# Kernel tuning notes

Measured on AMD Instinct MI355X. Metric: run time of the kernel, lower is better.

The kernel has to match this reference:

```python
import jax, jax.numpy as jnp
import numpy as np

DIM = 128
LAYERS = 3
N_NODES = 50000
N_EDGES = 640000
LN_EPS = 1e-5


def setup_inputs() -> dict:
    key = jax.random.key(0)
    ks = jax.random.split(key, 10)
    s = 1.0 / np.sqrt(DIM)
    x = jax.random.normal(ks[0], (N_NODES, DIM), dtype=jnp.float32)
    edge_index = jax.random.randint(ks[1], (2, N_EDGES), 0, N_NODES, dtype=jnp.int64)
    in_w = jax.random.uniform(ks[2], (DIM, DIM), jnp.float32, -s, s)
    in_b = jax.random.uniform(ks[3], (DIM,), jnp.float32, -s, s)
    w1 = jax.random.uniform(ks[4], (LAYERS, DIM, DIM), jnp.float32, -s, s)
    b1 = jax.random.uniform(ks[5], (LAYERS, DIM), jnp.float32, -s, s)
    w2 = jax.random.uniform(ks[6], (LAYERS, DIM, DIM), jnp.float32, -s, s)
    b2 = jax.random.uniform(ks[7], (LAYERS, DIM), jnp.float32, -s, s)
    ln_g = jnp.ones((LAYERS, DIM), jnp.float32)
    ln_b = jnp.zeros((LAYERS, DIM), jnp.float32)
    return {"x": x, "edge_index": edge_index, "in_w": in_w, "in_b": in_b,
            "w1": w1, "b1": b1, "w2": w2, "b2": b2, "ln_g": ln_g, "ln_b": ln_b}


def _layer_norm(z, g, b):
    mu = jnp.mean(z, axis=-1, keepdims=True)
    var = jnp.mean(jnp.square(z - mu), axis=-1, keepdims=True)
    return (z - mu) * jax.lax.rsqrt(var + LN_EPS) * g + b


def reference(x, edge_index, in_w, in_b, w1, b1, w2, b2, ln_g, ln_b):
    src, dst = edge_index[0], edge_index[1]
    n = x.shape[0]
    # degree is identical every layer in the original; compute once (same math)
    deg = jax.ops.segment_sum(jnp.ones(dst.shape, x.dtype), dst, num_segments=n)
    deg = jnp.maximum(deg, 1.0)[:, None]  # [N,1]
    h = x @ in_w + in_b  # [N,D]
    for i in range(w1.shape[0]):
        m = jax.ops.segment_sum(h[src], dst, num_segments=n) / deg  # gather+scatter
        mlp = jax.nn.relu(m @ w1[i] + b1[i]) @ w2[i] + b2[i]
        h = _layer_norm(h + mlp, ln_g[i], ln_b[i])
    return h
```

## Files before the change

kernel.cpp:

```cpp
#include <hip/hip_runtime.h>
#include <hip/hip_fp8.h>

#define DIM 128
#define LN_EPS 1e-5f
#define ECAP 512

typedef __attribute__((ext_vector_type(8))) short s16x8;
typedef __attribute__((ext_vector_type(4))) float f32x4;
typedef __attribute__((ext_vector_type(2))) float f32x2;
typedef __attribute__((ext_vector_type(4))) unsigned int u32x4;
typedef __attribute__((ext_vector_type(2))) unsigned int u32x2;

__device__ __forceinline__ unsigned short f2bf(float f) {
    unsigned u = __float_as_uint(f);
    unsigned r = u + 0x7fffu + ((u >> 16) & 1u);
    return (unsigned short)(r >> 16);
}
__device__ __forceinline__ float bf2f(unsigned short b) {
    return __uint_as_float(((unsigned)b) << 16);
}
__device__ __forceinline__ unsigned char f2fp8(float f) {
    return (unsigned char)__hip_cvt_float_to_fp8(f, __HIP_SATFINITE, __HIP_E4M3);
}
__device__ __forceinline__ void acc_fp8x4(float* a, unsigned v) {
    f32x2 lo = __builtin_amdgcn_cvt_pk_f32_fp8(v, false);
    f32x2 hi = __builtin_amdgcn_cvt_pk_f32_fp8(v, true);
    a[0] += lo[0]; a[1] += lo[1]; a[2] += hi[0]; a[3] += hi[1];
}


__global__ void count_deg(const int* __restrict__ dst, int E, int* __restrict__ counts) {
    int i = blockIdx.x * 256 + threadIdx.x;
    if (i < E) atomicAdd(&counts[dst[i]], 1);
}

__global__ __launch_bounds__(256) void scan_partials(const int* __restrict__ counts, int n,
                                                     int* __restrict__ bsum) {
    int base = blockIdx.x * 1024 + threadIdx.x * 4;
    int s = 0;
#pragma unroll
    for (int j = 0; j < 4; ++j) {
        int i = base + j;
        if (i < n) s += counts[i];
    }
#pragma unroll
    for (int off = 32; off > 0; off >>= 1) s += __shfl_xor(s, off, 64);
    __shared__ int wsum[4];
    int lane = threadIdx.x & 63, wid = threadIdx.x >> 6;
    if (lane == 0) wsum[wid] = s;
    __syncthreads();
    if (threadIdx.x == 0) bsum[blockIdx.x] = wsum[0] + wsum[1] + wsum[2] + wsum[3];
}

__global__ __launch_bounds__(64) void scan_bsums(const int* __restrict__ bsum,
                                                 int* __restrict__ bofs, int nb,
                                                 int* __restrict__ rowptr, int N, int E) {
    int lane = threadIdx.x;
    int carry = 0;
    for (int base = 0; base < nb; base += 64) {
        int v = (base + lane < nb) ? bsum[base + lane] : 0;
        int incl = v;
#pragma unroll
        for (int off = 1; off < 64; off <<= 1) {
            int t = __shfl_up(incl, off, 64);
            if (lane >= off) incl += t;
        }
        if (base + lane < nb) bofs[base + lane] = carry + incl - v;
        carry += __shfl(incl, 63, 64);
    }
    if (lane == 0) rowptr[N] = E;
}

__global__ __launch_bounds__(256) void scan_final(const int* __restrict__ counts, int n,
                                                  const int* __restrict__ bofs,
                                                  int* __restrict__ rowptr,
                                                  int* __restrict__ cursor,
                                                  float* __restrict__ dinv) {
    int base = blockIdx.x * 1024 + threadIdx.x * 4;
    int v[4];
#pragma unroll
    for (int j = 0; j < 4; ++j) {
        int i = base + j;
        v[j] = (i < n) ? counts[i] : 0;
    }
    int tsum = v[0] + v[1] + v[2] + v[3];
    int lane = threadIdx.x & 63, wid = threadIdx.x >> 6;
    int incl = tsum;
#pragma unroll
    for (int off = 1; off < 64; off <<= 1) {
        int t = __shfl_up(incl, off, 64);
        if (lane >= off) incl += t;
    }
    __shared__ int wsum[4];
    if (lane == 63) wsum[wid] = incl;
    __syncthreads();
    int wofs = 0;
    for (int w = 0; w < 4; ++w)
        if (w < wid) wofs += wsum[w];
    int excl = bofs[blockIdx.x] + wofs + (incl - tsum);
#pragma unroll
    for (int j = 0; j < 4; ++j) {
        int i = base + j;
        if (i < n) {
            rowptr[i] = excl;
            cursor[i] = excl;
            dinv[i] = 1.0f / (float)((v[j] > 1) ? v[j] : 1);
            excl += v[j];
        }
    }
}

__global__ void fill_csr(const int* __restrict__ src, const int* __restrict__ dst, int E,
                         int* __restrict__ cursor, int* __restrict__ srcidx) {
    int i = blockIdx.x * 256 + threadIdx.x;
    if (i < E) {
        int p = atomicAdd(&cursor[dst[i]], 1);
        srcidx[p] = src[i];
    }
}


__global__ __launch_bounds__(256) void cvt_weights(const float* __restrict__ in_w,
                                                   const float* __restrict__ w1,
                                                   const float* __restrict__ w2,
                                                   unsigned short* __restrict__ wt, int L) {
    int mat = blockIdx.x >> 3, part = blockIdx.x & 7;
    const float* src;
    if (mat == 0) src = in_w;
    else if (mat <= L) src = w1 + (size_t)(mat - 1) * DIM * DIM;
    else src = w2 + (size_t)(mat - 1 - L) * DIM * DIM;
    unsigned short* dst = wt + (size_t)mat * DIM * DIM;
    int base = part * 2048 + threadIdx.x;
#pragma unroll
    for (int j = 0; j < 8; ++j) {
        int i = base + j * 256;
        int k = i >> 7, n = i & 127;
        dst[n * DIM + k] = f2bf(src[i]);
    }
}


__global__ __launch_bounds__(256) void gemm_bias_mfma(const float* __restrict__ x,
                                                      const unsigned short* __restrict__ Wt,
                                                      const float* __restrict__ bias,
                                                      unsigned short* __restrict__ hb,
                                                      unsigned char* __restrict__ h8, int N) {
    int tid = threadIdx.x;
    int s = tid >> 6, lane = tid & 63;
    int quad = lane >> 4, l16 = lane & 15;
    int r0 = blockIdx.x * 16;
    int cs = s * 32;
    int arow = r0 + l16;
    bool av = arow < N;

    f32x4 acc[2];
    acc[0] = (f32x4){0.f, 0.f, 0.f, 0.f};
    acc[1] = (f32x4){0.f, 0.f, 0.f, 0.f};

    const float4* xp = (const float4*)(x + ((size_t)(av ? arow : 0) << 7)) + quad * 2;
#pragma unroll
    for (int k0 = 0; k0 < 128; k0 += 32) {
        s16x8 a = {0, 0, 0, 0, 0, 0, 0, 0};
        if (av) {
            float4 f0 = xp[k0 / 4];
            float4 f1 = xp[k0 / 4 + 1];
            a[0] = (short)f2bf(f0.x); a[1] = (short)f2bf(f0.y);
            a[2] = (short)f2bf(f0.z); a[3] = (short)f2bf(f0.w);
            a[4] = (short)f2bf(f1.x); a[5] = (short)f2bf(f1.y);
            a[6] = (short)f2bf(f1.z); a[7] = (short)f2bf(f1.w);
        }
        s16x8 b0 = *(const s16x8*)(Wt + ((size_t)(cs + l16) << 7) + quad * 8 + k0);
        s16x8 b1 = *(const s16x8*)(Wt + ((size_t)(cs + 16 + l16) << 7) + quad * 8 + k0);
        acc[0] = __builtin_amdgcn_mfma_f32_16x16x32_bf16(a, b0, acc[0], 0, 0, 0);
        acc[1] = __builtin_amdgcn_mfma_f32_16x16x32_bf16(a, b1, acc[1], 0, 0, 0);
    }

#pragma unroll
    for (int c = 0; c < 2; ++c) {
        int col = cs + c * 16 + l16;
        float bv = bias[col];
#pragma unroll
        for (int reg = 0; reg < 4; ++reg) {
            int grow = r0 + quad * 4 + reg;
            if (grow < N) {
                float o = acc[c][reg] + bv;
                hb[((size_t)grow << 7) + col] = f2bf(o);
                h8[((size_t)grow << 7) + col] = f2fp8(o);
            }
        }
    }
}


__global__ __launch_bounds__(256) void agg_mlp_ln(const unsigned short* __restrict__ hin,
                                                  const unsigned char* __restrict__ h8in,
                                                  const int* __restrict__ rowptr,
                                                  const int* __restrict__ srcidx,
                                                  const float* __restrict__ dinv,
                                                  const unsigned short* __restrict__ W1t,
                                                  const float* __restrict__ B1,
                                                  const unsigned short* __restrict__ W2t,
                                                  const float* __restrict__ B2,
                                                  const float* __restrict__ G,
                                                  const float* __restrict__ Bb,
                                                  unsigned short* __restrict__ hout,
                                                  unsigned char* __restrict__ h8out,
                                                  float* __restrict__ out_f32, int N) {
    __shared__ unsigned short M[16][132];
    __shared__ unsigned short P[16][132];
    __shared__ float s1p[4][16], s2p[4][16];
    __shared__ int eL[ECAP];
    __shared__ int rp[17];

    int tid = threadIdx.x;
    int s = tid >> 6, lane = tid & 63;
    int quad = lane >> 4, l16 = lane & 15;
    int g = lane >> 2, li = lane & 3;
    int r0 = blockIdx.x * 16;
    int cs = s * 32;

    if (tid < 17) {
        int idx = r0 + tid;
        rp[tid] = rowptr[idx < N ? idx : N];
    }
    __syncthreads();
    int ebase = rp[0];
    int etot = rp[16] - ebase;
    int estg = etot < ECAP ? etot : ECAP;
    for (int i = tid; i < estg; i += 256) eL[i] = srcidx[ebase + i];
    __syncthreads();

    int nd = r0 + g;
    bool nv = nd < N;
    int ls = rp[g] - ebase;
    int le = rp[g + 1] - ebase;
    if (!nv) { ls = 0; le = 0; }
    float di = nv ? dinv[nd] : 0.f;

    const unsigned char* hsl = h8in + cs + li * 8;

    float a0[8] = {0, 0, 0, 0, 0, 0, 0, 0};
    float a1[8] = {0, 0, 0, 0, 0, 0, 0, 0};

#define LIDX(jj) (((jj) < le) ? (((jj) < ECAP) ? eL[(jj)] : srcidx[ebase + (jj)]) : -1)

    int jA = ls;
    int iA0 = LIDX(jA + 0), iA1 = LIDX(jA + 1), iA2 = LIDX(jA + 2), iA3 = LIDX(jA + 3);
    u32x2 A0 = {0, 0}, A1 = {0, 0}, A2 = {0, 0}, A3 = {0, 0};
    if (iA0 >= 0) A0 = *(const u32x2*)(hsl + ((size_t)iA0 << 7));
    if (iA1 >= 0) A1 = *(const u32x2*)(hsl + ((size_t)iA1 << 7));
    if (iA2 >= 0) A2 = *(const u32x2*)(hsl + ((size_t)iA2 << 7));
    if (iA3 >= 0) A3 = *(const u32x2*)(hsl + ((size_t)iA3 << 7));
    int jB = jA + 4;
    int iB0 = LIDX(jB + 0), iB1 = LIDX(jB + 1), iB2 = LIDX(jB + 2), iB3 = LIDX(jB + 3);

    while (__any(jA < le)) {
        u32x2 B0 = {0, 0}, B1v = {0, 0}, B2v = {0, 0}, B3 = {0, 0};
        if (iB0 >= 0) B0  = *(const u32x2*)(hsl + ((size_t)iB0 << 7));
        if (iB1 >= 0) B1v = *(const u32x2*)(hsl + ((size_t)iB1 << 7));
        if (iB2 >= 0) B2v = *(const u32x2*)(hsl + ((size_t)iB2 << 7));
        if (iB3 >= 0) B3  = *(const u32x2*)(hsl + ((size_t)iB3 << 7));
        int jC = jB + 4;
        int iC0 = LIDX(jC + 0), iC1 = LIDX(jC + 1), iC2 = LIDX(jC + 2), iC3 = LIDX(jC + 3);
        acc_fp8x4(a0, A0[0]); acc_fp8x4(a0 + 4, A0[1]);
        acc_fp8x4(a1, A1[0]); acc_fp8x4(a1 + 4, A1[1]);
        acc_fp8x4(a0, A2[0]); acc_fp8x4(a0 + 4, A2[1]);
        acc_fp8x4(a1, A3[0]); acc_fp8x4(a1 + 4, A3[1]);
        jA = jB; A0 = B0; A1 = B1v; A2 = B2v; A3 = B3;
        jB = jC; iB0 = iC0; iB1 = iC1; iB2 = iC2; iB3 = iC3;
    }
#undef LIDX

    {
        u32x4 o;
#pragma unroll
        for (int j = 0; j < 4; ++j) {
            unsigned lo = f2bf((a0[2 * j]     + a1[2 * j])     * di);
            unsigned hi = f2bf((a0[2 * j + 1] + a1[2 * j + 1]) * di);
            o[j] = lo | (hi << 16);
        }
        *(u32x4*)(&M[g][cs + li * 8]) = o;
    }
    __syncthreads();

    unsigned short hvr[2][4];
#pragma unroll
    for (int c = 0; c < 2; ++c) {
        int col = cs + c * 16 + l16;
#pragma unroll
        for (int reg = 0; reg < 4; ++reg) {
            int grow = r0 + quad * 4 + reg;
            hvr[c][reg] = (grow < N) ? hin[((size_t)grow << 7) + col] : (unsigned short)0;
        }
    }

    f32x4 acc[2];
    acc[0] = (f32x4){0.f, 0.f, 0.f, 0.f};
    acc[1] = (f32x4){0.f, 0.f, 0.f, 0.f};
#pragma unroll
    for (int k0 = 0; k0 < 128; k0 += 32) {
        s16x8 a = *(const s16x8*)(&M[l16][quad * 8 + k0]);
        s16x8 b0 = *(const s16x8*)(W1t + ((size_t)(cs + l16) << 7) + quad * 8 + k0);
        s16x8 b1 = *(const s16x8*)(W1t + ((size_t)(cs + 16 + l16) << 7) + quad * 8 + k0);
        acc[0] = __builtin_amdgcn_mfma_f32_16x16x32_bf16(a, b0, acc[0], 0, 0, 0);
        acc[1] = __builtin_amdgcn_mfma_f32_16x16x32_bf16(a, b1, acc[1], 0, 0, 0);
    }
#pragma unroll
    for (int c = 0; c < 2; ++c) {
        int col = cs + c * 16 + l16;
        float bv = B1[col];
#pragma unroll
        for (int reg = 0; reg < 4; ++reg) {
            float v = fmaxf(acc[c][reg] + bv, 0.f);
            P[quad * 4 + reg][col] = f2bf(v);
        }
    }
    __syncthreads();

    acc[0] = (f32x4){0.f, 0.f, 0.f, 0.f};
    acc[1] = (f32x4){0.f, 0.f, 0.f, 0.f};
#pragma unroll
    for (int k0 = 0; k0 < 128; k0 += 32) {
        s16x8 a = *(const s16x8*)(&P[l16][quad * 8 + k0]);
        s16x8 b0 = *(const s16x8*)(W2t + ((size_t)(cs + l16) << 7) + quad * 8 + k0);
        s16x8 b1 = *(const s16x8*)(W2t + ((size_t)(cs + 16 + l16) << 7) + quad * 8 + k0);
        acc[0] = __builtin_amdgcn_mfma_f32_16x16x32_bf16(a, b0, acc[0], 0, 0, 0);
        acc[1] = __builtin_amdgcn_mfma_f32_16x16x32_bf16(a, b1, acc[1], 0, 0, 0);
    }

    float z[2][4];
    float ps1[4] = {0, 0, 0, 0}, ps2[4] = {0, 0, 0, 0};
#pragma unroll
    for (int c = 0; c < 2; ++c) {
        int col = cs + c * 16 + l16;
        float b2v = B2[col];
#pragma unroll
        for (int reg = 0; reg < 4; ++reg) {
            float hv = bf2f(hvr[c][reg]);
            float zz = acc[c][reg] + b2v + hv;
            z[c][reg] = zz;
            ps1[reg] += zz;
            ps2[reg] += zz * zz;
        }
    }
#pragma unroll
    for (int off = 1; off < 16; off <<= 1) {
#pragma unroll
        for (int reg = 0; reg < 4; ++reg) {
            ps1[reg] += __shfl_xor(ps1[reg], off, 64);
            ps2[reg] += __shfl_xor(ps2[reg], off, 64);
        }
    }
    if (l16 == 0) {
#pragma unroll
        for (int reg = 0; reg < 4; ++reg) {
            s1p[s][quad * 4 + reg] = ps1[reg];
            s2p[s][quad * 4 + reg] = ps2[reg];
        }
    }
    __syncthreads();

#pragma unroll
    for (int reg = 0; reg < 4; ++reg) {
        int row = quad * 4 + reg;
        float S1 = s1p[0][row] + s1p[1][row] + s1p[2][row] + s1p[3][row];
        float S2 = s2p[0][row] + s2p[1][row] + s2p[2][row] + s2p[3][row];
        float mean = S1 * (1.0f / 128.0f);
        float var = S2 * (1.0f / 128.0f) - mean * mean;
        float rs = rsqrtf(var + LN_EPS);
        int grow = r0 + row;
        if (grow < N) {
#pragma unroll
            for (int c = 0; c < 2; ++c) {
                int col = cs + c * 16 + l16;
                float o = (z[c][reg] - mean) * rs * G[col] + Bb[col];
                if (out_f32) {
                    out_f32[((size_t)grow << 7) + col] = o;
                } else {
                    hout[((size_t)grow << 7) + col] = f2bf(o);
                    h8out[((size_t)grow << 7) + col] = f2fp8(o);
                }
            }
        }
    }
}


extern "C" void kernel_launch(void* const* d_in, const int* in_sizes, int n_in,
                              void* d_out, int out_size, void* d_ws, size_t ws_size,
                              hipStream_t stream) {
    const float* x    = (const float*)d_in[0];
    const int*   ei   = (const int*)d_in[1];
    const float* in_w = (const float*)d_in[2];
    const float* in_b = (const float*)d_in[3];
    const float* w1   = (const float*)d_in[4];
    const float* b1   = (const float*)d_in[5];
    const float* w2   = (const float*)d_in[6];
    const float* b2   = (const float*)d_in[7];
    const float* ln_g = (const float*)d_in[8];
    const float* ln_b = (const float*)d_in[9];

    const int N = in_sizes[0] / DIM;
    const int E = in_sizes[1] / 2;
    const int LAYERS = in_sizes[4] / (DIM * DIM);

    const int* e_src = ei;
    const int* e_dst = ei + E;

    char* ws = (char*)d_ws;
    unsigned short* hb0    = (unsigned short*)ws;  ws += (size_t)N * DIM * 2;
    unsigned short* hb1    = (unsigned short*)ws;  ws += (size_t)N * DIM * 2;
    unsigned char*  h8a    = (unsigned char*)ws;   ws += (size_t)N * DIM;
    unsigned char*  h8b    = (unsigned char*)ws;   ws += (size_t)N * DIM;
    int*            counts = (int*)ws;             ws += (size_t)N * 4;
    int*            rowptr = (int*)ws;             ws += (size_t)(N + 1) * 4;
    int*            cursor = (int*)ws;             ws += (size_t)N * 4;
    float*          dinv   = (float*)ws;           ws += (size_t)N * 4;
    int*            srcidx = (int*)ws;             ws += (size_t)E * 4;
    int*            bsum   = (int*)ws;             ws += 4096;
    int*            bofs   = (int*)ws;             ws += 4096;
    unsigned short* wt     = (unsigned short*)ws;  ws += (size_t)(2 * LAYERS + 1) * DIM * DIM * 2;

    const int nScanBlocks = (N + 1023) / 1024;
    const int nMat = 2 * LAYERS + 1;

    (void)hipMemsetAsync(counts, 0, (size_t)N * 4, stream);
    count_deg<<<(E + 255) / 256, 256, 0, stream>>>(e_dst, E, counts);
    scan_partials<<<nScanBlocks, 256, 0, stream>>>(counts, N, bsum);
    scan_bsums<<<1, 64, 0, stream>>>(bsum, bofs, nScanBlocks, rowptr, N, E);
    scan_final<<<nScanBlocks, 256, 0, stream>>>(counts, N, bofs, rowptr, cursor, dinv);
    fill_csr<<<(E + 255) / 256, 256, 0, stream>>>(e_src, e_dst, E, cursor, srcidx);
    cvt_weights<<<nMat * 8, 256, 0, stream>>>(in_w, w1, w2, wt, LAYERS);

    const unsigned short* in_wt = wt;
    const unsigned short* w1t   = wt + (size_t)DIM * DIM;
    const unsigned short* w2t   = wt + (size_t)(1 + LAYERS) * DIM * DIM;

    int tile_grid = (N + 15) / 16;
    gemm_bias_mfma<<<tile_grid, 256, 0, stream>>>(x, in_wt, in_b, hb0, h8a, N);

    unsigned short* hin  = hb0;  unsigned char* h8in  = h8a;
    unsigned short* hout = hb1;  unsigned char* h8out = h8b;
    for (int i = 0; i < LAYERS; ++i) {
        float* out = (i == LAYERS - 1) ? (float*)d_out : nullptr;
        agg_mlp_ln<<<tile_grid, 256, 0, stream>>>(hin, h8in, rowptr, srcidx, dinv,
                                                  w1t + (size_t)i * DIM * DIM, b1 + (size_t)i * DIM,
                                                  w2t + (size_t)i * DIM * DIM, b2 + (size_t)i * DIM,
                                                  ln_g + (size_t)i * DIM, ln_b + (size_t)i * DIM,
                                                  hout, h8out, out, N);
        unsigned short* t = hin; hin = hout; hout = t;
        unsigned char* t8 = h8in; h8in = h8out; h8out = t8;
    }
}
```

Measured before the change: 353.8 us.

## Process 32 rows per block in fused aggregate-MLP-LN kernel with wider gathers

The fused aggregation+MLP+LayerNorm kernel now handles 32 node rows per block instead of 16. Each wave gathers 8 nodes, with 8 lanes per node loading 16-byte fp8 chunks, replacing the old scheme of 4 lanes per node loading 8 bytes. Each wave runs two 16-row MFMA tiles per weight fragment, so every W1/W2 fragment load is reused twice, and the shared edge-index staging capacity grows. Separately, the degree-count and CSR-fill kernels now process four edges per thread with int4 loads. This trades more registers and LDS per block, and fewer blocks, for better weight reuse and wider memory transactions.

```diff
diff --git a/kernel.cpp b/kernel.cpp
--- a/kernel.cpp
+++ b/kernel.cpp
@@ -3,7 +3,7 @@
 
 #define DIM 128
 #define LN_EPS 1e-5f
-#define ECAP 512
+#define ECAP 640
 
 typedef __attribute__((ext_vector_type(8))) short s16x8;
 typedef __attribute__((ext_vector_type(4))) float f32x4;
@@ -27,11 +27,25 @@
     f32x2 hi = __builtin_amdgcn_cvt_pk_f32_fp8(v, true);
     a[0] += lo[0]; a[1] += lo[1]; a[2] += hi[0]; a[3] += hi[1];
 }
+__device__ __forceinline__ void acc_fp8x16(float* a, u32x4 v) {
+    acc_fp8x4(a + 0,  v[0]);
+    acc_fp8x4(a + 4,  v[1]);
+    acc_fp8x4(a + 8,  v[2]);
+    acc_fp8x4(a + 12, v[3]);
+}
 
 
 __global__ void count_deg(const int* __restrict__ dst, int E, int* __restrict__ counts) {
-    int i = blockIdx.x * 256 + threadIdx.x;
-    if (i < E) atomicAdd(&counts[dst[i]], 1);
+    int i = (blockIdx.x * 256 + threadIdx.x) * 4;
+    if (i + 3 < E) {
+        int4 d = *(const int4*)(dst + i);
+        atomicAdd(&counts[d.x], 1);
+        atomicAdd(&counts[d.y], 1);
+        atomicAdd(&counts[d.z], 1);
+        atomicAdd(&counts[d.w], 1);
+    } else {
+        for (int j = i; j < E; ++j) atomicAdd(&counts[dst[j]], 1);
+    }
 }
 
 __global__ __launch_bounds__(256) void scan_partials(const int* __restrict__ counts, int n,
@@ -112,10 +126,19 @@
 
 __global__ void fill_csr(const int* __restrict__ src, const int* __restrict__ dst, int E,
                          int* __restrict__ cursor, int* __restrict__ srcidx) {
-    int i = blockIdx.x * 256 + threadIdx.x;
-    if (i < E) {
-        int p = atomicAdd(&cursor[dst[i]], 1);
-        srcidx[p] = src[i];
+    int i = (blockIdx.x * 256 + threadIdx.x) * 4;
+    if (i + 3 < E) {
+        int4 s = *(const int4*)(src + i);
+        int4 d = *(const int4*)(dst + i);
+        int p0 = atomicAdd(&cursor[d.x], 1); srcidx[p0] = s.x;
+        int p1 = atomicAdd(&cursor[d.y], 1); srcidx[p1] = s.y;
+        int p2 = atomicAdd(&cursor[d.z], 1); srcidx[p2] = s.z;
+        int p3 = atomicAdd(&cursor[d.w], 1); srcidx[p3] = s.w;
+    } else {
+        for (int j = i; j < E; ++j) {
+            int p = atomicAdd(&cursor[dst[j]], 1);
+            srcidx[p] = src[j];
+        }
     }
 }
 
@@ -206,179 +229,211 @@
                                                   unsigned short* __restrict__ hout,
                                                   unsigned char* __restrict__ h8out,
                                                   float* __restrict__ out_f32, int N) {
-    __shared__ unsigned short M[16][132];
-    __shared__ unsigned short P[16][132];
-    __shared__ float s1p[4][16], s2p[4][16];
+    __shared__ unsigned short M[32][132];
+    __shared__ unsigned short P[32][132];
+    __shared__ float s1p[4][32], s2p[4][32];
     __shared__ int eL[ECAP];
-    __shared__ int rp[17];
+    __shared__ int rp[33];
 
     int tid = threadIdx.x;
-    int s = tid >> 6, lane = tid & 63;
+    int w = tid >> 6, lane = tid & 63;
     int quad = lane >> 4, l16 = lane & 15;
-    int g = lane >> 2, li = lane & 3;
-    int r0 = blockIdx.x * 16;
-    int cs = s * 32;
-
-    if (tid < 17) {
+    int g = lane >> 3, li = lane & 7;
+    int r0 = blockIdx.x * 32;
+    int cs = w * 32;
+
+    if (tid < 33) {
         int idx = r0 + tid;
         rp[tid] = rowptr[idx < N ? idx : N];
     }
     __syncthreads();
     int ebase = rp[0];
-    int etot = rp[16] - ebase;
+    int etot = rp[32] - ebase;
     int estg = etot < ECAP ? etot : ECAP;
     for (int i = tid; i < estg; i += 256) eL[i] = srcidx[ebase + i];
     __syncthreads();
 
-    int nd = r0 + g;
+    int nrow = w * 8 + g;
+    int nd = r0 + nrow;
     bool nv = nd < N;
-    int ls = rp[g] - ebase;
-    int le = rp[g + 1] - ebase;
+    int ls = rp[nrow] - ebase;
+    int le = rp[nrow + 1] - ebase;
     if (!nv) { ls = 0; le = 0; }
     float di = nv ? dinv[nd] : 0.f;
 
-    const unsigned char* hsl = h8in + cs + li * 8;
-
-    float a0[8] = {0, 0, 0, 0, 0, 0, 0, 0};
-    float a1[8] = {0, 0, 0, 0, 0, 0, 0, 0};
+    const unsigned char* hsl = h8in + li * 16;
+
+    float a[16];
+#pragma unroll
+    for (int j = 0; j < 16; ++j) a[j] = 0.f;
 
 #define LIDX(jj) (((jj) < le) ? (((jj) < ECAP) ? eL[(jj)] : srcidx[ebase + (jj)]) : -1)
 
     int jA = ls;
     int iA0 = LIDX(jA + 0), iA1 = LIDX(jA + 1), iA2 = LIDX(jA + 2), iA3 = LIDX(jA + 3);
-    u32x2 A0 = {0, 0}, A1 = {0, 0}, A2 = {0, 0}, A3 = {0, 0};
-    if (iA0 >= 0) A0 = *(const u32x2*)(hsl + ((size_t)iA0 << 7));
-    if (iA1 >= 0) A1 = *(const u32x2*)(hsl + ((size_t)iA1 << 7));
-    if (iA2 >= 0) A2 = *(const u32x2*)(hsl + ((size_t)iA2 << 7));
-    if (iA3 >= 0) A3 = *(const u32x2*)(hsl + ((size_t)iA3 << 7));
+    u32x4 A0 = {0, 0, 0, 0}, A1 = {0, 0, 0, 0}, A2 = {0, 0, 0, 0}, A3 = {0, 0, 0, 0};
+    if (iA0 >= 0) A0 = *(const u32x4*)(hsl + ((size_t)iA0 << 7));
+    if (iA1 >= 0) A1 = *(const u32x4*)(hsl + ((size_t)iA1 << 7));
+    if (iA2 >= 0) A2 = *(const u32x4*)(hsl + ((size_t)iA2 << 7));
+    if (iA3 >= 0) A3 = *(const u32x4*)(hsl + ((size_t)iA3 << 7));
     int jB = jA + 4;
     int iB0 = LIDX(jB + 0), iB1 = LIDX(jB + 1), iB2 = LIDX(jB + 2), iB3 = LIDX(jB + 3);
 
     while (__any(jA < le)) {
-        u32x2 B0 = {0, 0}, B1v = {0, 0}, B2v = {0, 0}, B3 = {0, 0};
-        if (iB0 >= 0) B0  = *(const u32x2*)(hsl + ((size_t)iB0 << 7));
-        if (iB1 >= 0) B1v = *(const u32x2*)(hsl + ((size_t)iB1 << 7));
-        if (iB2 >= 0) B2v = *(const u32x2*)(hsl + ((size_t)iB2 << 7));
-        if (iB3 >= 0) B3  = *(const u32x2*)(hsl + ((size_t)iB3 << 7));
+        u32x4 B0 = {0, 0, 0, 0}, B1v = {0, 0, 0, 0}, B2v = {0, 0, 0, 0}, B3 = {0, 0, 0, 0};
+        if (iB0 >= 0) B0  = *(const u32x4*)(hsl + ((size_t)iB0 << 7));
+        if (iB1 >= 0) B1v = *(const u32x4*)(hsl + ((size_t)iB1 << 7));
+        if (iB2 >= 0) B2v = *(const u32x4*)(hsl + ((size_t)iB2 << 7));
+        if (iB3 >= 0) B3  = *(const u32x4*)(hsl + ((size_t)iB3 << 7));
         int jC = jB + 4;
         int iC0 = LIDX(jC + 0), iC1 = LIDX(jC + 1), iC2 = LIDX(jC + 2), iC3 = LIDX(jC + 3);
-        acc_fp8x4(a0, A0[0]); acc_fp8x4(a0 + 4, A0[1]);
-        acc_fp8x4(a1, A1[0]); acc_fp8x4(a1 + 4, A1[1]);
-        acc_fp8x4(a0, A2[0]); acc_fp8x4(a0 + 4, A2[1]);
-        acc_fp8x4(a1, A3[0]); acc_fp8x4(a1 + 4, A3[1]);
+        acc_fp8x16(a, A0);
+        acc_fp8x16(a, A1);
+        acc_fp8x16(a, A2);
+        acc_fp8x16(a, A3);
         jA = jB; A0 = B0; A1 = B1v; A2 = B2v; A3 = B3;
         jB = jC; iB0 = iC0; iB1 = iC1; iB2 = iC2; iB3 = iC3;
     }
 #undef LIDX
 
     {
-        u32x4 o;
+        u32x4 o0, o1;
 #pragma unroll
         for (int j = 0; j < 4; ++j) {
-            unsigned lo = f2bf((a0[2 * j]     + a1[2 * j])     * di);
-            unsigned hi = f2bf((a0[2 * j + 1] + a1[2 * j + 1]) * di);
-            o[j] = lo | (hi << 16);
-        }
-        *(u32x4*)(&M[g][cs + li * 8]) = o;
-    }
-    __syncthreads();
-
-    unsigned short hvr[2][4];
-#pragma unroll
-    for (int c = 0; c < 2; ++c) {
-        int col = cs + c * 16 + l16;
-#pragma unroll
-        for (int reg = 0; reg < 4; ++reg) {
-            int grow = r0 + quad * 4 + reg;
-            hvr[c][reg] = (grow < N) ? hin[((size_t)grow << 7) + col] : (unsigned short)0;
-        }
-    }
-
-    f32x4 acc[2];
-    acc[0] = (f32x4){0.f, 0.f, 0.f, 0.f};
-    acc[1] = (f32x4){0.f, 0.f, 0.f, 0.f};
+            unsigned lo0 = f2bf(a[2 * j]     * di);
+            unsigned hi0 = f2bf(a[2 * j + 1] * di);
+            o0[j] = lo0 | (hi0 << 16);
+            unsigned lo1 = f2bf(a[8 + 2 * j]     * di);
+            unsigned hi1 = f2bf(a[8 + 2 * j + 1] * di);
+            o1[j] = lo1 | (hi1 << 16);
+        }
+        *(u32x4*)(&M[nrow][li * 16])     = o0;
+        *(u32x4*)(&M[nrow][li * 16 + 8]) = o1;
+    }
+    __syncthreads();
+
+    unsigned short hvr[2][2][4];
+#pragma unroll
+    for (int rt = 0; rt < 2; ++rt) {
+#pragma unroll
+        for (int c = 0; c < 2; ++c) {
+            int col = cs + c * 16 + l16;
+#pragma unroll
+            for (int reg = 0; reg < 4; ++reg) {
+                int grow = r0 + rt * 16 + quad * 4 + reg;
+                hvr[rt][c][reg] = (grow < N) ? hin[((size_t)grow << 7) + col] : (unsigned short)0;
+            }
+        }
+    }
+
+    f32x4 ac1[2][2];
+    ac1[0][0] = (f32x4){0.f, 0.f, 0.f, 0.f}; ac1[0][1] = (f32x4){0.f, 0.f, 0.f, 0.f};
+    ac1[1][0] = (f32x4){0.f, 0.f, 0.f, 0.f}; ac1[1][1] = (f32x4){0.f, 0.f, 0.f, 0.f};
 #pragma unroll
     for (int k0 = 0; k0 < 128; k0 += 32) {
-        s16x8 a = *(const s16x8*)(&M[l16][quad * 8 + k0]);
         s16x8 b0 = *(const s16x8*)(W1t + ((size_t)(cs + l16) << 7) + quad * 8 + k0);
         s16x8 b1 = *(const s16x8*)(W1t + ((size_t)(cs + 16 + l16) << 7) + quad * 8 + k0);
-        acc[0] = __builtin_amdgcn_mfma_f32_16x16x32_bf16(a, b0, acc[0], 0, 0, 0);
-        acc[1] = __builtin_amdgcn_mfma_f32_16x16x32_bf16(a, b1, acc[1], 0, 0, 0);
-    }
-#pragma unroll
-    for (int c = 0; c < 2; ++c) {
-        int col = cs + c * 16 + l16;
-        float bv = B1[col];
-#pragma unroll
-        for (int reg = 0; reg < 4; ++reg) {
-            float v = fmaxf(acc[c][reg] + bv, 0.f);
-            P[quad * 4 + reg][col] = f2bf(v);
-        }
-    }
-    __syncthreads();
-
-    acc[0] = (f32x4){0.f, 0.f, 0.f, 0.f};
-    acc[1] = (f32x4){0.f, 0.f, 0.f, 0.f};
+        s16x8 a0 = *(const s16x8*)(&M[l16][quad * 8 + k0]);
+        s16x8 a1 = *(const s16x8*)(&M[16 + l16][quad * 8 + k0]);
+        ac1[0][0] = __builtin_amdgcn_mfma_f32_16x16x32_bf16(a0, b0, ac1[0][0], 0, 0, 0);
+        ac1[0][1] = __builtin_amdgcn_mfma_f32_16x16x32_bf16(a0, b1, ac1[0][1], 0, 0, 0);
+        ac1[1][0] = __builtin_amdgcn_mfma_f32_16x16x32_bf16(a1, b0, ac1[1][0], 0, 0, 0);
+        ac1[1][1] = __builtin_amdgcn_mfma_f32_16x16x32_bf16(a1, b1, ac1[1][1], 0, 0, 0);
+    }
+#pragma unroll
+    for (int rt = 0; rt < 2; ++rt) {
+#pragma unroll
+        for (int c = 0; c < 2; ++c) {
+            int col = cs + c * 16 + l16;
+            float bv = B1[col];
+#pragma unroll
+            for (int reg = 0; reg < 4; ++reg) {
+                float v = fmaxf(ac1[rt][c][reg] + bv, 0.f);
+                P[rt * 16 + quad * 4 + reg][col] = f2bf(v);
+            }
+        }
+    }
+    __syncthreads();
+
+    f32x4 ac2[2][2];
+    ac2[0][0] = (f32x4){0.f, 0.f, 0.f, 0.f}; ac2[0][1] = (f32x4){0.f, 0.f, 0.f, 0.f};
+    ac2[1][0] = (f32x4){0.f, 0.f, 0.f, 0.f}; ac2[1][1] = (f32x4){0.f, 0.f, 0.f, 0.f};
 #pragma unroll
     for (int k0 = 0; k0 < 128; k0 += 32) {
-        s16x8 a = *(const s16x8*)(&P[l16][quad * 8 + k0]);
         s16x8 b0 = *(const s16x8*)(W2t + ((size_t)(cs + l16) << 7) + quad * 8 + k0);
         s16x8 b1 = *(const s16x8*)(W2t + ((size_t)(cs + 16 + l16) << 7) + quad * 8 + k0);
-        acc[0] = __builtin_amdgcn_mfma_f32_16x16x32_bf16(a, b0, acc[0], 0, 0, 0);
-        acc[1] = __builtin_amdgcn_mfma_f32_16x16x32_bf16(a, b1, acc[1], 0, 0, 0);
-    }
-
-    float z[2][4];
-    float ps1[4] = {0, 0, 0, 0}, ps2[4] = {0, 0, 0, 0};
-#pragma unroll
-    for (int c = 0; c < 2; ++c) {
-        int col = cs + c * 16 + l16;
-        float b2v = B2[col];
+        s16x8 a0 = *(const s16x8*)(&P[l16][quad * 8 + k0]);
+        s16x8 a1 = *(const s16x8*)(&P[16 + l16][quad * 8 + k0]);
+        ac2[0][0] = __builtin_amdgcn_mfma_f32_16x16x32_bf16(a0, b0, ac2[0][0], 0, 0, 0);
+        ac2[0][1] = __builtin_amdgcn_mfma_f32_16x16x32_bf16(a0, b1, ac2[0][1], 0, 0, 0);
+        ac2[1][0] = __builtin_amdgcn_mfma_f32_16x16x32_bf16(a1, b0, ac2[1][0], 0, 0, 0);
+        ac2[1][1] = __builtin_amdgcn_mfma_f32_16x16x32_bf16(a1, b1, ac2[1][1], 0, 0, 0);
+    }
+
+    float z[2][2][4];
+    float ps1[2][4] = {{0, 0, 0, 0}, {0, 0, 0, 0}};
+    float ps2[2][4] = {{0, 0, 0, 0}, {0, 0, 0, 0}};
+#pragma unroll
+    for (int rt = 0; rt < 2; ++rt) {
+#pragma unroll
+        for (int c = 0; c < 2; ++c) {
+            int col = cs + c * 16 + l16;
+            float b2v = B2[col];
+#pragma unroll
+            for (int reg = 0; reg < 4; ++reg) {
+                float hv = bf2f(hvr[rt][c][reg]);
+                float zz = ac2[rt][c][reg] + b2v + hv;
+                z[rt][c][reg] = zz;
+                ps1[rt][reg] += zz;
+                ps2[rt][reg] += zz * zz;
+            }
+        }
+    }
+#pragma unroll
+    for (int off = 1; off < 16; off <<= 1) {
+#pragma unroll
+        for (int rt = 0; rt < 2; ++rt) {
+#pragma unroll
+            for (int reg = 0; reg < 4; ++reg) {
+                ps1[rt][reg] += __shfl_xor(ps1[rt][reg], off, 64);
+                ps2[rt][reg] += __shfl_xor(ps2[rt][reg], off, 64);
+            }
+        }
+    }
+    if (l16 == 0) {
+#pragma unroll
+        for (int rt = 0; rt < 2; ++rt) {
+#pragma unroll
+            for (int reg = 0; reg < 4; ++reg) {
+                s1p[w][rt * 16 + quad * 4 + reg] = ps1[rt][reg];
+                s2p[w][rt * 16 + quad * 4 + reg] = ps2[rt][reg];
+            }
+        }
+    }
+    __syncthreads();
+
+#pragma unroll
+    for (int rt = 0; rt < 2; ++rt) {
 #pragma unroll
         for (int reg = 0; reg < 4; ++reg) {
-            float hv = bf2f(hvr[c][reg]);
-            float zz = acc[c][reg] + b2v + hv;
-            z[c][reg] = zz;
-            ps1[reg] += zz;
-            ps2[reg] += zz * zz;
-        }
-    }
-#pragma unroll
-    for (int off = 1; off < 16; off <<= 1) {
-#pragma unroll
-        for (int reg = 0; reg < 4; ++reg) {
-            ps1[reg] += __shfl_xor(ps1[reg], off, 64);
-            ps2[reg] += __shfl_xor(ps2[reg], off, 64);
-        }
-    }
-    if (l16 == 0) {
-#pragma unroll
-        for (int reg = 0; reg < 4; ++reg) {
-            s1p[s][quad * 4 + reg] = ps1[reg];
-            s2p[s][quad * 4 + reg] = ps2[reg];
-        }
-    }
-    __syncthreads();
-
-#pragma unroll
-    for (int reg = 0; reg < 4; ++reg) {
-        int row = quad * 4 + reg;
-        float S1 = s1p[0][row] + s1p[1][row] + s1p[2][row] + s1p[3][row];
-        float S2 = s2p[0][row] + s2p[1][row] + s2p[2][row] + s2p[3][row];
-        float mean = S1 * (1.0f / 128.0f);
-        float var = S2 * (1.0f / 128.0f) - mean * mean;
-        float rs = rsqrtf(var + LN_EPS);
-        int grow = r0 + row;
-        if (grow < N) {
-#pragma unroll
-            for (int c = 0; c < 2; ++c) {
-                int col = cs + c * 16 + l16;
-                float o = (z[c][reg] - mean) * rs * G[col] + Bb[col];
-                if (out_f32) {
-                    out_f32[((size_t)grow << 7) + col] = o;
-                } else {
-                    hout[((size_t)grow << 7) + col] = f2bf(o);
-                    h8out[((size_t)grow << 7) + col] = f2fp8(o);
+            int row = rt * 16 + quad * 4 + reg;
+            float S1 = s1p[0][row] + s1p[1][row] + s1p[2][row] + s1p[3][row];
+            float S2 = s2p[0][row] + s2p[1][row] + s2p[2][row] + s2p[3][row];
+            float mean = S1 * (1.0f / 128.0f);
+            float var = S2 * (1.0f / 128.0f) - mean * mean;
+            float rs = rsqrtf(var + LN_EPS);
+            int grow = r0 + row;
+            if (grow < N) {
+#pragma unroll
+                for (int c = 0; c < 2; ++c) {
+                    int col = cs + c * 16 + l16;
+                    float o = (z[rt][c][reg] - mean) * rs * G[col] + Bb[col];
+                    if (out_f32) {
+                        out_f32[((size_t)grow << 7) + col] = o;
+                    } else {
+                        hout[((size_t)grow << 7) + col] = f2bf(o);
+                        h8out[((size_t)grow << 7) + col] = f2fp8(o);
+                    }
                 }
             }
         }
@@ -425,29 +480,29 @@
     const int nMat = 2 * LAYERS + 1;
 
     (void)hipMemsetAsync(counts, 0, (size_t)N * 4, stream);
-    count_deg<<<(E + 255) / 256, 256, 0, stream>>>(e_dst, E, counts);
+    count_deg<<<(E + 1023) / 1024, 256, 0, stream>>>(e_dst, E, counts);
     scan_partials<<<nScanBlocks, 256, 0, stream>>>(counts, N, bsum);
     scan_bsums<<<1, 64, 0, stream>>>(bsum, bofs, nScanBlocks, rowptr, N, E);
     scan_final<<<nScanBlocks, 256, 0, stream>>>(counts, N, bofs, rowptr, cursor, dinv);
-    fill_csr<<<(E + 255) / 256, 256, 0, stream>>>(e_src, e_dst, E, cursor, srcidx);
+    fill_csr<<<(E + 1023) / 1024, 256, 0, stream>>>(e_src, e_dst, E, cursor, srcidx);
     cvt_weights<<<nMat * 8, 256, 0, stream>>>(in_w, w1, w2, wt, LAYERS);
 
     const unsigned short* in_wt = wt;
     const unsigned short* w1t   = wt + (size_t)DIM * DIM;
     const unsigned short* w2t   = wt + (size_t)(1 + LAYERS) * DIM * DIM;
 
-    int tile_grid = (N + 15) / 16;
-    gemm_bias_mfma<<<tile_grid, 256, 0, stream>>>(x, in_wt, in_b, hb0, h8a, N);
-
+    gemm_bias_mfma<<<(N + 15) / 16, 256, 0, stream>>>(x, in_wt, in_b, hb0, h8a, N);
+
+    int agg_grid = (N + 31) / 32;
     unsigned short* hin  = hb0;  unsigned char* h8in  = h8a;
     unsigned short* hout = hb1;  unsigned char* h8out = h8b;
     for (int i = 0; i < LAYERS; ++i) {
         float* out = (i == LAYERS - 1) ? (float*)d_out : nullptr;
-        agg_mlp_ln<<<tile_grid, 256, 0, stream>>>(hin, h8in, rowptr, srcidx, dinv,
-                                                  w1t + (size_t)i * DIM * DIM, b1 + (size_t)i * DIM,
-                                                  w2t + (size_t)i * DIM * DIM, b2 + (size_t)i * DIM,
-                                                  ln_g + (size_t)i * DIM, ln_b + (size_t)i * DIM,
-                                                  hout, h8out, out, N);
+        agg_mlp_ln<<<agg_grid, 256, 0, stream>>>(hin, h8in, rowptr, srcidx, dinv,
+                                                 w1t + (size_t)i * DIM * DIM, b1 + (size_t)i * DIM,
+                                                 w2t + (size_t)i * DIM * DIM, b2 + (size_t)i * DIM,
+                                                 ln_g + (size_t)i * DIM, ln_b + (size_t)i * DIM,
+                                                 hout, h8out, out, N);
         unsigned short* t = hin; hin = hout; hout = t;
         unsigned char* t8 = h8in; h8in = h8out; h8out = t8;
     }
```

After: 357.8 us. No clear change (+1.1%).
